# Optimization experiments

Measured on AMD Instinct MI355X. Metric: run time of the kernel, lower is better.

Reference implementation:

```python
import jax, jax.numpy as jnp
import numpy as np

B, N, F_IN, F_OUT = 8, 2048, 512, 512


def setup_inputs() -> dict:
    key = jax.random.key(0)
    k1, k2, k3, k4 = jax.random.split(key, 4)
    X = jax.random.normal(k1, (B, N, F_IN), dtype=jnp.float32)
    A = jax.random.uniform(k2, (B, N, N), dtype=jnp.float32)
    # nn.Linear params (kaiming-uniform-ish scale is irrelevant for correctness)
    bound = 1.0 / np.sqrt(F_IN)
    W = jax.random.uniform(k3, (F_IN, F_OUT), dtype=jnp.float32, minval=-bound, maxval=bound)
    b = jax.random.uniform(k4, (F_OUT,), dtype=jnp.float32, minval=-bound, maxval=bound)
    return {"X": X, "A": A, "W": W, "b": b}


def reference(X, A, W, b):
    # A' = A + I  (self-loops)
    A_hat = A + jnp.eye(A.shape[-1], dtype=A.dtype)
    # D^{-1/2}: per-row degree of A'.  torch builds diag_embed + two bmms;
    # mathematically identical to broadcasted row/column scaling.
    d_inv_sqrt = A_hat.sum(axis=-1) ** -0.5                      # [B, N]
    L = A_hat * d_inv_sqrt[:, :, None] * d_inv_sqrt[:, None, :]  # [B, N, N]
    x = X @ W + b                                                # [B, N, F_out]
    return jnp.einsum('bij,bjf->bif', L, x)
```

## Files before the change

kernel.cpp:

```cpp
#include <hip/hip_runtime.h>

#define B_ 8
#define N_ 2048
#define FIN_ 512
#define FOUT_ 512

typedef __attribute__((ext_vector_type(8))) short short8;
typedef __attribute__((ext_vector_type(4))) float floatx4;
typedef __attribute__((ext_vector_type(4))) unsigned short ushortx4;
typedef __attribute__((ext_vector_type(8))) unsigned short ushortx8;

__device__ inline unsigned short f2bf(float f) {
    union { float f; unsigned int u; } x; x.f = f;
    unsigned int r = x.u + 0x7FFFu + ((x.u >> 16) & 1u);
    return (unsigned short)(r >> 16);
}

__device__ inline void glds16(const void* g, void* l) {
    __builtin_amdgcn_global_load_lds(
        (const __attribute__((address_space(1))) void*)g,
        (__attribute__((address_space(3))) void*)l, 16, 0, 0);
}

__global__ __launch_bounds__(256) void degree_kernel(const float* __restrict__ A,
                                                     float* __restrict__ dinv) {
    int row = blockIdx.x;
    const float4* A4 = (const float4*)(A + (size_t)row * N_);
    int t = threadIdx.x;
    float4 v0 = A4[t];
    float4 v1 = A4[t + 256];
    float s = v0.x + v0.y + v0.z + v0.w + v1.x + v1.y + v1.z + v1.w;
#pragma unroll
    for (int off = 32; off > 0; off >>= 1) s += __shfl_down(s, off, 64);
    __shared__ float red[4];
    if ((t & 63) == 0) red[t >> 6] = s;
    __syncthreads();
    if (t == 0) dinv[row] = rsqrtf(red[0] + red[1] + red[2] + red[3] + 1.0f);
}

__global__ __launch_bounds__(256) void scaleL_kernel(const float* __restrict__ A,
                                                     const float* __restrict__ dinv,
                                                     unsigned short* __restrict__ Lbf) {
    size_t e0 = ((size_t)blockIdx.x * 256 + threadIdx.x) * 8;
    int b   = (int)(e0 >> 22);
    int rem = (int)(e0 & ((1u << 22) - 1));
    int i   = rem >> 11;
    int j0  = rem & 2047;
    float di = dinv[b * N_ + i];
    const float* dj = dinv + b * N_ + j0;
    float4 a0 = *(const float4*)(A + e0);
    float4 a1 = *(const float4*)(A + e0 + 4);
    float4 d0 = *(const float4*)(dj);
    float4 d1 = *(const float4*)(dj + 4);
    float av[8] = {a0.x, a0.y, a0.z, a0.w, a1.x, a1.y, a1.z, a1.w};
    float dv[8] = {d0.x, d0.y, d0.z, d0.w, d1.x, d1.y, d1.z, d1.w};
    int dd = i - j0;
    if (dd >= 0 && dd < 8) av[dd] += 1.0f;
    ushortx8 p;
#pragma unroll
    for (int r = 0; r < 8; ++r) p[r] = f2bf(av[r] * di * dv[r]);
    *(ushortx8*)(Lbf + e0) = p;
}

__global__ __launch_bounds__(256) void castX_kernel(const float* __restrict__ X,
                                                    unsigned short* __restrict__ Xbf) {
    size_t e0 = ((size_t)blockIdx.x * 256 + threadIdx.x) * 8;
    float4 a0 = *(const float4*)(X + e0);
    float4 a1 = *(const float4*)(X + e0 + 4);
    float av[8] = {a0.x, a0.y, a0.z, a0.w, a1.x, a1.y, a1.z, a1.w};
    ushortx8 p;
#pragma unroll
    for (int r = 0; r < 8; ++r) p[r] = f2bf(av[r]);
    *(ushortx8*)(Xbf + e0) = p;
}

__global__ __launch_bounds__(256) void transposeW_kernel(const float* __restrict__ W,
                                                         unsigned short* __restrict__ Wt) {
    __shared__ float tile[32][33];
    int bx = blockIdx.x * 32;
    int by = blockIdx.y * 32;
    int tx = threadIdx.x, ty = threadIdx.y;
#pragma unroll
    for (int r = 0; r < 32; r += 8)
        tile[ty + r][tx] = W[(size_t)(by + ty + r) * FOUT_ + bx + tx];
    __syncthreads();
#pragma unroll
    for (int r = 0; r < 32; r += 8)
        Wt[(size_t)(bx + ty + r) * FIN_ + by + tx] = f2bf(tile[tx][ty + r]);
}


__global__ __launch_bounds__(256) void gemm1_kernel(
    const unsigned short* __restrict__ Abase,
    const unsigned short* __restrict__ Btbase,
    unsigned short* __restrict__ XwT,
    const float* __restrict__ bias) {
    __shared__ __align__(16) char smem[34816];
    char* As = smem;
    char* Bs = smem + 16384;

    int t = threadIdx.x;
    int lane = t & 63;
    int wave = t >> 6;
    int wr = wave >> 1, wc = wave & 1;
    int q = lane >> 4, m = lane & 15;
    int n0 = blockIdx.x * 128;
    int m0 = blockIdx.y * 128;

    int srow = t >> 3;
    int scol = (((t & 7) ^ (srow & 7)) * 8);
    int x0 = ((q ^ (m & 7)) * 16);
    int x1 = x0 ^ 64;

    floatx4 acc[4][4];
#pragma unroll
    for (int mi = 0; mi < 4; ++mi)
#pragma unroll
        for (int ni = 0; ni < 4; ++ni)
            acc[mi][ni] = (floatx4){0.f, 0.f, 0.f, 0.f};

    const unsigned short* gA = Abase + (size_t)(m0 + srow) * FIN_ + scol;
    const unsigned short* gB = Btbase + (size_t)(n0 + srow) * FIN_ + scol;
    char* lA = As + wave * 1024;
    char* lB = Bs + wave * 1024;

    for (int kt = 0; kt < FIN_ / 64; ++kt) {
#pragma unroll
        for (int u = 0; u < 4; ++u) {
            glds16(gA + (size_t)(u * 32) * FIN_, lA + u * 4096);
            glds16(gB + (size_t)(u * 32) * FIN_, lB + u * 4096);
        }
        gA += 64; gB += 64;
        __syncthreads();

#pragma unroll
        for (int sl = 0; sl < 2; ++sl) {
            int xs = sl ? x1 : x0;
            short8 af[4], bfr[4];
#pragma unroll
            for (int mi = 0; mi < 4; ++mi)
                af[mi] = *(const short8*)(As + (wr * 64 + mi * 16 + m) * 128 + xs);
#pragma unroll
            for (int ni = 0; ni < 4; ++ni)
                bfr[ni] = *(const short8*)(Bs + (wc * 64 + ni * 16 + m) * 128 + xs);
#pragma unroll
            for (int mi = 0; mi < 4; ++mi)
#pragma unroll
                for (int ni = 0; ni < 4; ++ni)
                    acc[mi][ni] = __builtin_amdgcn_mfma_f32_16x16x32_bf16(
                        af[mi], bfr[ni], acc[mi][ni], 0, 0, 0);
        }
        __syncthreads();
    }

    unsigned short* T = (unsigned short*)smem;
#pragma unroll
    for (int mi = 0; mi < 4; ++mi) {
        int row = wr * 64 + mi * 16 + q * 4;
#pragma unroll
        for (int ni = 0; ni < 4; ++ni) {
            int col = wc * 64 + ni * 16 + m;
            float bv = bias[n0 + col];
            ushortx4 pk;
#pragma unroll
            for (int r = 0; r < 4; ++r) pk[r] = f2bf(acc[mi][ni][r] + bv);
            *(ushortx4*)(T + col * 136 + row) = pk;
        }
    }
    __syncthreads();
    int f  = t >> 1;
    int c0 = (t & 1) * 64;
    int bb = m0 >> 11;
    int node0 = (m0 & 2047) + c0;
    unsigned short* dst = XwT + ((size_t)bb * FOUT_ + n0 + f) * N_ + node0;
    const unsigned short* src = T + f * 136 + c0;
#pragma unroll
    for (int u = 0; u < 8; ++u)
        *(ushortx8*)(dst + u * 8) = *(const ushortx8*)(src + u * 8);
}

__global__ __launch_bounds__(256) void gemm2_kernel(
    const unsigned short* __restrict__ Lbf,
    const unsigned short* __restrict__ XwT,
    float* __restrict__ out) {
    __shared__ __align__(16) char smem[32768];
    char* As = smem;
    char* Bs = smem + 16384;

    int t = threadIdx.x;
    int lane = t & 63;
    int wave = t >> 6;
    int wr = wave >> 1, wc = wave & 1;
    int q = lane >> 4, m = lane & 15;

    int id = blockIdx.x;
    int b  = id & 7;
    int s  = id >> 3;
    int n0 = (s & 3) * 128;
    int m0 = (s >> 2) * 128;

    const unsigned short* Ab = Lbf + (size_t)b * N_ * N_;
    const unsigned short* Bb = XwT + (size_t)b * FOUT_ * N_;

    int srow = t >> 3;
    int scol = (((t & 7) ^ (srow & 7)) * 8);
    int x0 = ((q ^ (m & 7)) * 16);
    int x1 = x0 ^ 64;

    floatx4 acc[4][4];
#pragma unroll
    for (int mi = 0; mi < 4; ++mi)
#pragma unroll
        for (int ni = 0; ni < 4; ++ni)
            acc[mi][ni] = (floatx4){0.f, 0.f, 0.f, 0.f};

    const unsigned short* gA = Ab + (size_t)(m0 + srow) * N_ + scol;
    const unsigned short* gB = Bb + (size_t)(n0 + srow) * N_ + scol;
    char* lA = As + wave * 1024;
    char* lB = Bs + wave * 1024;

    for (int kt = 0; kt < N_ / 64; ++kt) {
#pragma unroll
        for (int u = 0; u < 4; ++u) {
            glds16(gA + (size_t)(u * 32) * N_, lA + u * 4096);
            glds16(gB + (size_t)(u * 32) * N_, lB + u * 4096);
        }
        gA += 64; gB += 64;
        __syncthreads();

#pragma unroll
        for (int sl = 0; sl < 2; ++sl) {
            int xs = sl ? x1 : x0;
            short8 af[4], bfr[4];
#pragma unroll
            for (int mi = 0; mi < 4; ++mi)
                af[mi] = *(const short8*)(As + (wr * 64 + mi * 16 + m) * 128 + xs);
#pragma unroll
            for (int ni = 0; ni < 4; ++ni)
                bfr[ni] = *(const short8*)(Bs + (wc * 64 + ni * 16 + m) * 128 + xs);
#pragma unroll
            for (int mi = 0; mi < 4; ++mi)
#pragma unroll
                for (int ni = 0; ni < 4; ++ni)
                    acc[mi][ni] = __builtin_amdgcn_mfma_f32_16x16x32_bf16(
                        af[mi], bfr[ni], acc[mi][ni], 0, 0, 0);
        }
        __syncthreads();
    }

    float* C = out + (size_t)b * N_ * FOUT_;
#pragma unroll
    for (int mi = 0; mi < 4; ++mi) {
        int rowb = m0 + wr * 64 + mi * 16 + q * 4;
#pragma unroll
        for (int ni = 0; ni < 4; ++ni) {
            int col = n0 + wc * 64 + ni * 16 + m;
#pragma unroll
            for (int r = 0; r < 4; ++r)
                C[(size_t)(rowb + r) * FOUT_ + col] = acc[mi][ni][r];
        }
    }
}

extern "C" void kernel_launch(void* const* d_in, const int* in_sizes, int n_in,
                              void* d_out, int out_size, void* d_ws, size_t ws_size,
                              hipStream_t stream) {
    const float* X    = (const float*)d_in[0];
    const float* A    = (const float*)d_in[1];
    const float* W    = (const float*)d_in[2];
    const float* bias = (const float*)d_in[3];
    float* out = (float*)d_out;
    char* ws = (char*)d_ws;

    float* dinv          = (float*)(ws);
    unsigned short* Xbf  = (unsigned short*)(ws + (1u << 16));
    unsigned short* Wt   = (unsigned short*)(ws + (1u << 16) + 16777216u);
    unsigned short* XwT  = (unsigned short*)(ws + (1u << 16) + 16777216u + 524288u);
    unsigned short* Lbf  = (unsigned short*)(ws + (1u << 16) + 16777216u + 524288u + 16777216u);

    degree_kernel<<<B_ * N_, 256, 0, stream>>>(A, dinv);
    scaleL_kernel<<<(B_ * (size_t)N_ * N_) / 2048, 256, 0, stream>>>(A, dinv, Lbf);
    castX_kernel<<<((size_t)B_ * N_ * FIN_) / 2048, 256, 0, stream>>>(X, Xbf);
    transposeW_kernel<<<dim3(FOUT_ / 32, FIN_ / 32), dim3(32, 8), 0, stream>>>(W, Wt);

    gemm1_kernel<<<dim3(FOUT_ / 128, (B_ * N_) / 128), 256, 0, stream>>>(
        Xbf, Wt, XwT, bias);

    gemm2_kernel<<<512, 256, 0, stream>>>(Lbf, XwT, out);
}
```

Baseline: 328.4 us.

## Fold degree scaling into GEMM epilogues and fuse A cast with degree pass

Removes the separate pass that builds the normalized L matrix. The degree kernel now also writes a bf16 copy of raw A. The column scaling by d^-1/2 moves into the gemm1 epilogue, and the row scaling plus the identity term (adding the scaled y row) move into the gemm2 epilogue. This drops one full read of the 128MB fp32 A and one 64MB bf16 write. The cost is an extra scattered bf16 read of XwT in the gemm2 epilogue, and bf16 rounding that now happens on raw A instead of on L, which may shift accuracy slightly.

```diff
diff --git a/kernel.cpp b/kernel.cpp
--- a/kernel.cpp
+++ b/kernel.cpp
@@ -22,13 +22,20 @@
         (__attribute__((address_space(3))) void*)l, 16, 0, 0);
 }
 
-__global__ __launch_bounds__(256) void degree_kernel(const float* __restrict__ A,
-                                                     float* __restrict__ dinv) {
+__global__ __launch_bounds__(256) void degree_cast_kernel(
+    const float* __restrict__ A, float* __restrict__ dinv,
+    unsigned short* __restrict__ Abf) {
     int row = blockIdx.x;
-    const float4* A4 = (const float4*)(A + (size_t)row * N_);
+    size_t base = (size_t)row * N_;
+    const float4* A4 = (const float4*)(A + base);
     int t = threadIdx.x;
     float4 v0 = A4[t];
     float4 v1 = A4[t + 256];
+    ushortx4 p0, p1;
+    p0[0] = f2bf(v0.x); p0[1] = f2bf(v0.y); p0[2] = f2bf(v0.z); p0[3] = f2bf(v0.w);
+    p1[0] = f2bf(v1.x); p1[1] = f2bf(v1.y); p1[2] = f2bf(v1.z); p1[3] = f2bf(v1.w);
+    *(ushortx4*)(Abf + base + t * 4) = p0;
+    *(ushortx4*)(Abf + base + (t + 256) * 4) = p1;
     float s = v0.x + v0.y + v0.z + v0.w + v1.x + v1.y + v1.z + v1.w;
 #pragma unroll
     for (int off = 32; off > 0; off >>= 1) s += __shfl_down(s, off, 64);
@@ -36,30 +43,6 @@
     if ((t & 63) == 0) red[t >> 6] = s;
     __syncthreads();
     if (t == 0) dinv[row] = rsqrtf(red[0] + red[1] + red[2] + red[3] + 1.0f);
-}
-
-__global__ __launch_bounds__(256) void scaleL_kernel(const float* __restrict__ A,
-                                                     const float* __restrict__ dinv,
-                                                     unsigned short* __restrict__ Lbf) {
-    size_t e0 = ((size_t)blockIdx.x * 256 + threadIdx.x) * 8;
-    int b   = (int)(e0 >> 22);
-    int rem = (int)(e0 & ((1u << 22) - 1));
-    int i   = rem >> 11;
-    int j0  = rem & 2047;
-    float di = dinv[b * N_ + i];
-    const float* dj = dinv + b * N_ + j0;
-    float4 a0 = *(const float4*)(A + e0);
-    float4 a1 = *(const float4*)(A + e0 + 4);
-    float4 d0 = *(const float4*)(dj);
-    float4 d1 = *(const float4*)(dj + 4);
-    float av[8] = {a0.x, a0.y, a0.z, a0.w, a1.x, a1.y, a1.z, a1.w};
-    float dv[8] = {d0.x, d0.y, d0.z, d0.w, d1.x, d1.y, d1.z, d1.w};
-    int dd = i - j0;
-    if (dd >= 0 && dd < 8) av[dd] += 1.0f;
-    ushortx8 p;
-#pragma unroll
-    for (int r = 0; r < 8; ++r) p[r] = f2bf(av[r] * di * dv[r]);
-    *(ushortx8*)(Lbf + e0) = p;
 }
 
 __global__ __launch_bounds__(256) void castX_kernel(const float* __restrict__ X,
@@ -94,7 +77,8 @@
     const unsigned short* __restrict__ Abase,
     const unsigned short* __restrict__ Btbase,
     unsigned short* __restrict__ XwT,
-    const float* __restrict__ bias) {
+    const float* __restrict__ bias,
+    const float* __restrict__ dinv) {
     __shared__ __align__(16) char smem[34816];
     char* As = smem;
     char* Bs = smem + 16384;
@@ -157,13 +141,15 @@
 #pragma unroll
     for (int mi = 0; mi < 4; ++mi) {
         int row = wr * 64 + mi * 16 + q * 4;
+        float4 dv = *(const float4*)(dinv + m0 + row);
+        float dr[4] = {dv.x, dv.y, dv.z, dv.w};
 #pragma unroll
         for (int ni = 0; ni < 4; ++ni) {
             int col = wc * 64 + ni * 16 + m;
             float bv = bias[n0 + col];
             ushortx4 pk;
 #pragma unroll
-            for (int r = 0; r < 4; ++r) pk[r] = f2bf(acc[mi][ni][r] + bv);
+            for (int r = 0; r < 4; ++r) pk[r] = f2bf((acc[mi][ni][r] + bv) * dr[r]);
             *(ushortx4*)(T + col * 136 + row) = pk;
         }
     }
@@ -180,8 +166,9 @@
 }
 
 __global__ __launch_bounds__(256) void gemm2_kernel(
-    const unsigned short* __restrict__ Lbf,
+    const unsigned short* __restrict__ Abf,
     const unsigned short* __restrict__ XwT,
+    const float* __restrict__ dinv,
     float* __restrict__ out) {
     __shared__ __align__(16) char smem[32768];
     char* As = smem;
@@ -199,7 +186,7 @@
     int n0 = (s & 3) * 128;
     int m0 = (s >> 2) * 128;
 
-    const unsigned short* Ab = Lbf + (size_t)b * N_ * N_;
+    const unsigned short* Ab = Abf + (size_t)b * N_ * N_;
     const unsigned short* Bb = XwT + (size_t)b * FOUT_ * N_;
 
     int srow = t >> 3;
@@ -252,12 +239,17 @@
 #pragma unroll
     for (int mi = 0; mi < 4; ++mi) {
         int rowb = m0 + wr * 64 + mi * 16 + q * 4;
+        float4 dv = *(const float4*)(dinv + b * N_ + rowb);
+        float dr[4] = {dv.x, dv.y, dv.z, dv.w};
 #pragma unroll
         for (int ni = 0; ni < 4; ++ni) {
             int col = n0 + wc * 64 + ni * 16 + m;
-#pragma unroll
-            for (int r = 0; r < 4; ++r)
-                C[(size_t)(rowb + r) * FOUT_ + col] = acc[mi][ni][r];
+            ushortx4 yv = *(const ushortx4*)(Bb + (size_t)col * N_ + rowb);
+#pragma unroll
+            for (int r = 0; r < 4; ++r) {
+                union { unsigned int u; float f; } yc; yc.u = ((unsigned int)yv[r]) << 16;
+                C[(size_t)(rowb + r) * FOUT_ + col] = dr[r] * (acc[mi][ni][r] + yc.f);
+            }
         }
     }
 }
@@ -276,15 +268,14 @@
     unsigned short* Xbf  = (unsigned short*)(ws + (1u << 16));
     unsigned short* Wt   = (unsigned short*)(ws + (1u << 16) + 16777216u);
     unsigned short* XwT  = (unsigned short*)(ws + (1u << 16) + 16777216u + 524288u);
-    unsigned short* Lbf  = (unsigned short*)(ws + (1u << 16) + 16777216u + 524288u + 16777216u);
-
-    degree_kernel<<<B_ * N_, 256, 0, stream>>>(A, dinv);
-    scaleL_kernel<<<(B_ * (size_t)N_ * N_) / 2048, 256, 0, stream>>>(A, dinv, Lbf);
+    unsigned short* Abf  = (unsigned short*)(ws + (1u << 16) + 16777216u + 524288u + 16777216u);
+
+    degree_cast_kernel<<<B_ * N_, 256, 0, stream>>>(A, dinv, Abf);
     castX_kernel<<<((size_t)B_ * N_ * FIN_) / 2048, 256, 0, stream>>>(X, Xbf);
     transposeW_kernel<<<dim3(FOUT_ / 32, FIN_ / 32), dim3(32, 8), 0, stream>>>(W, Wt);
 
     gemm1_kernel<<<dim3(FOUT_ / 128, (B_ * N_) / 128), 256, 0, stream>>>(
-        Xbf, Wt, XwT, bias);
-
-    gemm2_kernel<<<512, 256, 0, stream>>>(Lbf, XwT, out);
-}
+        Xbf, Wt, XwT, bias, dinv);
+
+    gemm2_kernel<<<512, 256, 0, stream>>>(Abf, XwT, dinv, out);
+}
```

Result: faster. 289.1 us (-12.0%).
